# Kernel optimization log

Measured on AMD Instinct MI355X. Metric: run time of the kernel, lower is better.

Reference implementation:

```python
import jax, jax.numpy as jnp
import numpy as np

N = 100000
E = 1600000
IN_CH = 128
HID = 128
HEADS = 4
C = HID // HEADS  # 32 per-head channels
NUM_CLASSES = 40
NEG_SLOPE = 0.2


def _glorot(key, shape):
    fan_in, fan_out = shape[0], shape[-1]
    lim = jnp.sqrt(6.0 / (fan_in + fan_out))
    return jax.random.uniform(key, shape, jnp.float32, -lim, lim)


def setup_inputs() -> dict:
    key = jax.random.key(0)
    ks = jax.random.split(key, 12)
    x = jax.random.normal(ks[0], (N, IN_CH), jnp.float32)
    edge_index = jax.random.randint(ks[1], (2, E), 0, N, jnp.int64)
    edge_weight = jax.random.uniform(ks[2], (E,), jnp.float32)
    return {
        'x': x,
        'edge_index': edge_index,
        'edge_weight': edge_weight,
        'W_pre': _glorot(ks[3], (IN_CH, HID)),
        'Wl': _glorot(ks[4], (HID, HEADS * C)),
        'bl': jnp.zeros((HEADS * C,), jnp.float32),
        'Wr': _glorot(ks[5], (HID, HEADS * C)),
        'br': jnp.zeros((HEADS * C,), jnp.float32),
        'We': _glorot(ks[6], (1, HEADS * C)),
        'att': _glorot(ks[7], (HEADS, C)),
        'b_gat': jnp.zeros((HEADS * C,), jnp.float32),
        'W1': _glorot(ks[8], (HID, HID)),
        'b1': jnp.zeros((HID,), jnp.float32),
        'W2': _glorot(ks[9], (HID, NUM_CLASSES)),
        'b2': jnp.zeros((NUM_CLASSES,), jnp.float32),
    }


def reference(x, edge_index, edge_weight, W_pre, Wl, bl, Wr, br, We, att, b_gat, W1, b1, W2, b2):
    # pre projection (bias=False), norm = Identity
    h0 = x @ W_pre  # [N, HID]

    # --- GATv2Conv (PyG semantics, eval mode) ---
    # add self loops; self-loop edge_attr = mean of existing edge_attr (fill_value='mean')
    loop = jnp.arange(N, dtype=edge_index.dtype)
    src = jnp.concatenate([edge_index[0], loop])  # [E+N]
    dst = jnp.concatenate([edge_index[1], loop])
    ea = jnp.concatenate([edge_weight, jnp.full((N,), jnp.mean(edge_weight), edge_weight.dtype)])  # [E+N]

    x_l = (h0 @ Wl + bl).reshape(N, HEADS, C)  # source transform
    x_r = (h0 @ Wr + br).reshape(N, HEADS, C)  # target transform
    edge_emb = (ea[:, None] * We).reshape(-1, HEADS, C)  # lin_edge (bias=False)

    xj = x_l[src]  # [Etot, H, C] gather of source features
    e = jax.nn.leaky_relu(xj + x_r[dst] + edge_emb, NEG_SLOPE)
    alpha = jnp.einsum('ehc,hc->eh', e, att)  # [Etot, H]

    # segment softmax over destination neighborhoods
    amax = jax.ops.segment_max(alpha, dst, num_segments=N)
    amax = jnp.where(jnp.isfinite(amax), amax, 0.0)
    ex = jnp.exp(alpha - amax[dst])
    denom = jax.ops.segment_sum(ex, dst, num_segments=N)
    attn = ex / (denom[dst] + 1e-16)  # [Etot, H]

    out = jax.ops.segment_sum(attn[:, :, None] * xj, dst, num_segments=N)  # [N, H, C]
    out = out.reshape(N, HEADS * C) + b_gat

    h1 = jax.nn.elu(out)
    h = h0 + h1  # residual

    logits = jax.nn.relu(h @ W1 + b1) @ W2 + b2
    return h, logits
```

## Files before the change

### kernel.cpp

```cpp
#include <hip/hip_runtime.h>

typedef __attribute__((ext_vector_type(8))) short short8;
typedef __attribute__((ext_vector_type(16))) float f32x16;

#if __has_builtin(__builtin_amdgcn_exp2f)
#define EXP2(x) __builtin_amdgcn_exp2f(x)
#else
#define EXP2(x) exp2f(x)
#endif

static __device__ __forceinline__ unsigned short f2bf(float f){
  unsigned u = __float_as_uint(f);
  unsigned r = u + 0x7fffu + ((u >> 16) & 1u);
  return (unsigned short)(r >> 16);
}
static __device__ __forceinline__ float bf2f(unsigned short h){
  return __uint_as_float(((unsigned)h) << 16);
}

__global__ void wprep(const float* __restrict__ Wpre, const float* __restrict__ W1,
                      const float* __restrict__ W2, const float* __restrict__ bl,
                      const float* __restrict__ br,
                      unsigned short* __restrict__ PhiF, unsigned short* __restrict__ PloF,
                      unsigned short* __restrict__ W1hiF, unsigned short* __restrict__ W1loF,
                      unsigned short* __restrict__ W2hiF, unsigned short* __restrict__ W2loF,
                      float* __restrict__ bcat){
  int i = blockIdx.x*256 + threadIdx.x;
  float v; unsigned short* hp; unsigned short* lp; size_t idx;
  if (i < 16384){
    int k = i >> 7, c = i & 127;
    v = Wpre[i]; hp = PhiF; lp = PloF;
    idx = ((size_t)(k>>3)*128 + c)*8 + (k&7);
  } else if (i < 32768){
    int j = i - 16384; int k = j >> 7, c = j & 127;
    v = W1[j]; hp = W1hiF; lp = W1loF;
    idx = ((size_t)(k>>3)*128 + c)*8 + (k&7);
  } else if (i < 37888){
    int j = i - 32768; int k = j / 40, c = j % 40;
    v = W2[j]; hp = W2hiF; lp = W2loF;
    idx = ((size_t)(k>>3)*40 + c)*8 + (k&7);
  } else if (i < 38144){
    int j = i - 37888;
    bcat[j] = (j < 128) ? bl[j] : br[j-128];
    return;
  } else return;
  unsigned short h = f2bf(v);
  hp[idx] = h;
  lp[idx] = f2bf(v - bf2f(h));
}

__global__ __launch_bounds__(256) void wcomb_kernel(
    const float* __restrict__ Wpre, const float* __restrict__ Wl,
    const float* __restrict__ Wr,
    unsigned short* __restrict__ ChiF, unsigned short* __restrict__ CloF){
  int tid = blockIdx.x*256 + threadIdx.x;
  int r = tid >> 8;
  int c = tid & 255;
  const float* B = (c < 128) ? (Wl + c) : (Wr + (c - 128));
  float s = 0.f;
  for (int k = 0; k < 128; ++k)
    s = fmaf(Wpre[r*128 + k], B[(size_t)k*128], s);
  unsigned short h = f2bf(s);
  size_t idx = ((size_t)(r>>3)*256 + c)*8 + (r&7);
  ChiF[idx] = h;
  CloF[idx] = f2bf(s - bf2f(h));
}

__global__ void count_mean(const int* __restrict__ ei, const float* __restrict__ ew,
                           int* __restrict__ deg, int* __restrict__ rk,
                           float* __restrict__ msum, int E){
  float s = 0.f;
  for (int e = blockIdx.x*256 + threadIdx.x; e < E; e += gridDim.x*256){
    rk[e] = atomicAdd(&deg[ei[E + e]], 1);
    s += ew[e];
  }
  for (int d = 32; d > 0; d >>= 1) s += __shfl_down(s, d, 64);
  __shared__ float ps[4];
  int lane = threadIdx.x & 63, w = threadIdx.x >> 6;
  if (lane == 0) ps[w] = s;
  __syncthreads();
  if (threadIdx.x == 0) atomicAdd(msum, (ps[0]+ps[1]+ps[2]+ps[3]) / (float)E);
}

__global__ __launch_bounds__(256) void scan1_kernel(const int* __restrict__ deg, int* __restrict__ rowptr,
                                                    int* __restrict__ bsum, int* __restrict__ dhist, int N){
  __shared__ int s[256];
  __shared__ int lhist[256];
  int i = blockIdx.x*256 + threadIdx.x;
  lhist[threadIdx.x] = 0;
  __syncthreads();
  int v = (i < N) ? deg[i] : 0;
  if (i < N) atomicAdd(&lhist[v < 255 ? v : 255], 1);
  s[threadIdx.x] = v;
  __syncthreads();
  for (int off = 1; off < 256; off <<= 1){
    int t = (threadIdx.x >= off) ? s[threadIdx.x - off] : 0;
    __syncthreads();
    s[threadIdx.x] += t;
    __syncthreads();
  }
  if (i < N) rowptr[i + 1] = s[threadIdx.x];
  if (threadIdx.x == 255) bsum[blockIdx.x] = s[255];
  int c = lhist[threadIdx.x];
  if (c > 0) atomicAdd(&dhist[threadIdx.x], c);
}

__global__ __launch_bounds__(512) void scan2_kernel(const int* __restrict__ bsum, int* __restrict__ boff, int nb,
                                                    const int* __restrict__ dhist, int* __restrict__ dhoff){
  __shared__ int s[512];
  __shared__ int s2[256];
  int v = (threadIdx.x < nb) ? bsum[threadIdx.x] : 0;
  s[threadIdx.x] = v;
  __syncthreads();
  for (int off = 1; off < 512; off <<= 1){
    int t = (threadIdx.x >= off) ? s[threadIdx.x - off] : 0;
    __syncthreads();
    s[threadIdx.x] += t;
    __syncthreads();
  }
  if (threadIdx.x < nb) boff[threadIdx.x] = s[threadIdx.x] - v;
  int v2 = 0;
  if (threadIdx.x < 256){ v2 = dhist[threadIdx.x]; s2[threadIdx.x] = v2; }
  __syncthreads();
  for (int off = 1; off < 256; off <<= 1){
    int t = 0;
    if (threadIdx.x < 256 && threadIdx.x >= off) t = s2[threadIdx.x - off];
    __syncthreads();
    if (threadIdx.x < 256) s2[threadIdx.x] += t;
    __syncthreads();
  }
  if (threadIdx.x < 256) dhoff[threadIdx.x] = s2[threadIdx.x] - v2;
}

__global__ __launch_bounds__(256) void scan3_kernel(int* __restrict__ rowptr, const int* __restrict__ boff,
                                                    const int* __restrict__ deg, int* __restrict__ dhoff,
                                                    int* __restrict__ perm, int N){
  __shared__ int lcnt[256];
  __shared__ int lbase[256];
  int i = blockIdx.x*256 + threadIdx.x;
  lcnt[threadIdx.x] = 0;
  __syncthreads();
  if (i == 0) rowptr[0] = 0;
  int d = 0, lr = 0;
  if (i < N){
    rowptr[i + 1] += boff[i >> 8];
    d = deg[i]; d = d < 255 ? d : 255;
    lr = atomicAdd(&lcnt[d], 1);
  }
  __syncthreads();
  int c = lcnt[threadIdx.x];
  if (c > 0) lbase[threadIdx.x] = atomicAdd(&dhoff[threadIdx.x], c);
  __syncthreads();
  if (i < N) perm[lbase[d] + lr] = i;
}

__global__ void fill_kernel(const int* __restrict__ ei, const float* __restrict__ ew,
                            const int* __restrict__ rowptr, const int* __restrict__ rk,
                            int2* __restrict__ erec, int E){
  int e = blockIdx.x*256 + threadIdx.x;
  if (e >= E) return;
  int dst = ei[E + e];
  erec[rowptr[dst] + rk[e]] = make_int2(ei[e], __float_as_int(ew[e]));
}

template<int NT>
static __device__ __forceinline__ void stageA(short* alds, const float* __restrict__ A,
                                              int row0, int N, int t){
  for (int g = t; g < 1024; g += NT){
    int r = g >> 4, k8 = g & 15;
    int grow = row0 + r;
    float4 p0, p1;
    if (grow < N){
      const float* ap = A + (size_t)grow*128 + k8*8;
      p0 = *(const float4*)ap;
      p1 = *(const float4*)(ap + 4);
    } else {
      p0 = make_float4(0.f,0.f,0.f,0.f); p1 = p0;
    }
    float vv[8] = {p0.x,p0.y,p0.z,p0.w,p1.x,p1.y,p1.z,p1.w};
    short8 hv, lv;
    #pragma unroll
    for (int j = 0; j < 8; ++j){
      unsigned short h = f2bf(vv[j]);
      hv[j] = (short)h;
      lv[j] = (short)f2bf(vv[j] - bf2f(h));
    }
    int slot = k8 ^ (r & 15);
    *(short8*)&alds[r*128 + slot*8] = hv;
    *(short8*)&alds[8192 + r*128 + slot*8] = lv;
  }
}

#define MFMA_KLOOP(ACC0, ACC1) \
  _Pragma("unroll") \
  for (int ks = 0; ks < 8; ++ks){ \
    int k8 = ks*2 + kg; \
    const short* a0 = &alds[r0*128 + (k8 ^ sx)*8]; \
    const short* a1 = &alds[(r0+32)*128 + (k8 ^ sx)*8]; \
    short8 a0h = *(const short8*)a0; \
    short8 a0l = *(const short8*)(a0 + 8192); \
    short8 a1h = *(const short8*)a1; \
    short8 a1l = *(const short8*)(a1 + 8192); \
    ACC0 = __builtin_amdgcn_mfma_f32_32x32x16_bf16(a0h, bh[ks],  ACC0, 0,0,0); \
    ACC1 = __builtin_amdgcn_mfma_f32_32x32x16_bf16(a1h, bh[ks],  ACC1, 0,0,0); \
    ACC0 = __builtin_amdgcn_mfma_f32_32x32x16_bf16(a0l, bh[ks],  ACC0, 0,0,0); \
    ACC1 = __builtin_amdgcn_mfma_f32_32x32x16_bf16(a1l, bh[ks],  ACC1, 0,0,0); \
    ACC0 = __builtin_amdgcn_mfma_f32_32x32x16_bf16(a0h, bl8[ks], ACC0, 0,0,0); \
    ACC1 = __builtin_amdgcn_mfma_f32_32x32x16_bf16(a1h, bl8[ks], ACC1, 0,0,0); \
  }

__global__ __launch_bounds__(768) void pre_kernel(
    const float* __restrict__ A,
    const unsigned short* __restrict__ PhiF, const unsigned short* __restrict__ PloF,
    const unsigned short* __restrict__ ChiF, const unsigned short* __restrict__ CloF,
    const float* __restrict__ bcat,
    float* __restrict__ hout, unsigned short* __restrict__ xlr, int N, int ntiles)
{
  __shared__ short sh[2][16384];
  const int t = threadIdx.x;
  const int lane = t & 63, w = t >> 6;
  const int cl = lane & 31, kg = lane >> 5;
  const int sx = cl & 15;
  const int S = w * 32;
  const bool isP = S < 128;
  const int col = isP ? (S + cl) : (S - 128 + cl);
  const int NC  = isP ? 128 : 256;
  const unsigned short* Bhi = isP ? PhiF : ChiF;
  const unsigned short* Blo = isP ? PloF : CloF;
  const float bv = isP ? 0.f : bcat[col];

  short8 bh[8], bl8[8];
  #pragma unroll
  for (int ks = 0; ks < 8; ++ks){
    size_t off = ((size_t)(ks*2 + kg)*NC + col)*8;
    bh[ks]  = *(const short8*)(Bhi + off);
    bl8[ks] = *(const short8*)(Blo + off);
  }

  const int r_0 = t >> 4,         k8_0 = t & 15;
  const int g1  = t + 768;
  const int r_1 = g1 >> 4,        k8_1 = g1 & 15;
  const bool has1 = g1 < 1024;
  float4 pa0, pa1, pb0, pb1;

  auto LOAD = [&](int tl){
    int row0 = tl*64;
    int gr = row0 + r_0;
    if (gr < N){ const float* ap = A + (size_t)gr*128 + k8_0*8; pa0 = *(const float4*)ap; pa1 = *(const float4*)(ap+4); }
    else { pa0 = make_float4(0.f,0.f,0.f,0.f); pa1 = pa0; }
    if (has1){
      int gr1 = row0 + r_1;
      if (gr1 < N){ const float* ap = A + (size_t)gr1*128 + k8_1*8; pb0 = *(const float4*)ap; pb1 = *(const float4*)(ap+4); }
      else { pb0 = make_float4(0.f,0.f,0.f,0.f); pb1 = pb0; }
    }
  };
  auto STORE = [&](short* buf){
    {
      float vv[8] = {pa0.x,pa0.y,pa0.z,pa0.w,pa1.x,pa1.y,pa1.z,pa1.w};
      short8 hv, lv;
      #pragma unroll
      for (int j = 0; j < 8; ++j){
        unsigned short h = f2bf(vv[j]);
        hv[j] = (short)h;
        lv[j] = (short)f2bf(vv[j] - bf2f(h));
      }
      int slot = k8_0 ^ (r_0 & 15);
      *(short8*)&buf[r_0*128 + slot*8] = hv;
      *(short8*)&buf[8192 + r_0*128 + slot*8] = lv;
    }
    if (has1){
      float vv[8] = {pb0.x,pb0.y,pb0.z,pb0.w,pb1.x,pb1.y,pb1.z,pb1.w};
      short8 hv, lv;
      #pragma unroll
      for (int j = 0; j < 8; ++j){
        unsigned short h = f2bf(vv[j]);
        hv[j] = (short)h;
        lv[j] = (short)f2bf(vv[j] - bf2f(h));
      }
      int slot = k8_1 ^ (r_1 & 15);
      *(short8*)&buf[r_1*128 + slot*8] = hv;
      *(short8*)&buf[8192 + r_1*128 + slot*8] = lv;
    }
  };
  auto COMPUTE = [&](int tl, const short* alds){
    f32x16 acc0, acc1;
    #pragma unroll
    for (int i = 0; i < 16; ++i){ acc0[i] = 0.f; acc1[i] = 0.f; }
    const int r0 = cl;
    MFMA_KLOOP(acc0, acc1)
    int row0 = tl*64;
    if (isP){
      #pragma unroll
      for (int rt2 = 0; rt2 < 2; ++rt2){
        const f32x16& ac = rt2 ? acc1 : acc0;
        #pragma unroll
        for (int reg = 0; reg < 16; ++reg){
          int row = rt2*32 + (reg & 3) + 8*(reg >> 2) + 4*kg;
          int grow = row0 + row;
          if (grow < N) hout[(size_t)grow*128 + col] = ac[reg];
        }
      }
    } else {
      #pragma unroll
      for (int rt2 = 0; rt2 < 2; ++rt2){
        const f32x16& ac = rt2 ? acc1 : acc0;
        #pragma unroll
        for (int reg = 0; reg < 16; ++reg){
          int row = rt2*32 + (reg & 3) + 8*(reg >> 2) + 4*kg;
          int grow = row0 + row;
          if (grow < N) xlr[(size_t)grow*256 + col] = f2bf(ac[reg] + bv);
        }
      }
    }
  };

  int tile = blockIdx.x;
  if (tile >= ntiles) return;
  LOAD(tile);
  STORE(sh[0]);
  __syncthreads();
  int cur = 0;
  while (true){
    int next = tile + gridDim.x;
    bool more = next < ntiles;
    if (more) LOAD(next);
    COMPUTE(tile, sh[cur]);
    if (!more) break;
    STORE(sh[cur^1]);
    __syncthreads();
    cur ^= 1;
    tile = next;
  }
}

__global__ __launch_bounds__(256) void mlp_kernel(
    const float* __restrict__ A,
    const unsigned short* __restrict__ B1hi, const unsigned short* __restrict__ B1lo,
    const float* __restrict__ b1,
    const unsigned short* __restrict__ B2hi, const unsigned short* __restrict__ B2lo,
    const float* __restrict__ b2,
    float* __restrict__ logits, int N)
{
  __shared__ short alds[2*64*128];
  const int t = threadIdx.x;
  const int row0 = blockIdx.x * 64;
  stageA<256>(alds, A, row0, N, t);
  __syncthreads();

  const int lane = t & 63, w = t >> 6;
  const int cl = lane & 31, kg = lane >> 5;
  const int r0 = cl;
  const int sx = r0 & 15;

  {
    const int col = w*32 + cl;
    short8 bh[8], bl8[8];
    #pragma unroll
    for (int ks = 0; ks < 8; ++ks){
      size_t off = ((size_t)(ks*2 + kg)*128 + col)*8;
      bh[ks]  = *(const short8*)(B1hi + off);
      bl8[ks] = *(const short8*)(B1lo + off);
    }
    f32x16 acc0, acc1;
    #pragma unroll
    for (int i = 0; i < 16; ++i){ acc0[i] = 0.f; acc1[i] = 0.f; }
    MFMA_KLOOP(acc0, acc1)

    float bv = b1[col];
    __syncthreads();
    #pragma unroll
    for (int rt = 0; rt < 2; ++rt){
      const f32x16& ac = rt ? acc1 : acc0;
      #pragma unroll
      for (int reg = 0; reg < 16; ++reg){
        int row = rt*32 + (reg & 3) + 8*(reg >> 2) + 4*kg;
        float v = fmaxf(ac[reg] + bv, 0.f);
        unsigned short h = f2bf(v);
        unsigned short l = f2bf(v - bf2f(h));
        int idx = row*128 + (((col >> 3) ^ (row & 15)) << 3) + (col & 7);
        alds[idx] = (short)h;
        alds[8192 + idx] = (short)l;
      }
    }
    __syncthreads();
  }

  if (w < 2){
    const int col = w*32 + cl;
    const bool cok = col < 40;
    short8 bh[8], bl8[8];
    #pragma unroll
    for (int ks = 0; ks < 8; ++ks){
      if (cok){
        size_t off = ((size_t)(ks*2 + kg)*40 + col)*8;
        bh[ks]  = *(const short8*)(B2hi + off);
        bl8[ks] = *(const short8*)(B2lo + off);
      } else {
        #pragma unroll
        for (int j = 0; j < 8; ++j){ bh[ks][j] = 0; bl8[ks][j] = 0; }
      }
    }
    f32x16 acc0, acc1;
    #pragma unroll
    for (int i = 0; i < 16; ++i){ acc0[i] = 0.f; acc1[i] = 0.f; }
    MFMA_KLOOP(acc0, acc1)

    if (cok){
      float bv = b2[col];
      #pragma unroll
      for (int rt = 0; rt < 2; ++rt){
        const f32x16& ac = rt ? acc1 : acc0;
        #pragma unroll
        for (int reg = 0; reg < 16; ++reg){
          int row = rt*32 + (reg & 3) + 8*(reg >> 2) + 4*kg;
          int grow = row0 + row;
          if (grow < N) logits[(size_t)grow*40 + col] = ac[reg] + bv;
        }
      }
    }
  }
}

__global__ __launch_bounds__(256) void gather_kernel(
    const int* __restrict__ rowptr, const int2* __restrict__ erec,
    const unsigned short* __restrict__ xlr,
    const int* __restrict__ perm,
    const float* __restrict__ We, const float* __restrict__ att,
    const float* __restrict__ msum, const float* __restrict__ bgat,
    float* __restrict__ hbuf, int N)
{
  const int wid  = threadIdx.x >> 6;
  const int lane = threadIdx.x & 63;
  const int g    = lane >> 4;
  const int l    = lane & 15;
  const int ch0  = l * 8;
  const int slot = (blockIdx.x*4 + wid)*4 + g;
  const bool nok = slot < N;
  const int n    = nok ? perm[slot] : 0;

  float xrv[8], wev[8], at6[8], at4[8];
  {
    short8 q = *(const short8*)&xlr[(size_t)n*256 + 128 + ch0];
    float4 w0 = *(const float4*)&We[ch0];
    float4 w1 = *(const float4*)&We[ch0+4];
    float4 a0 = *(const float4*)&att[ch0];
    float4 a1 = *(const float4*)&att[ch0+4];
    const float L2E = 1.4426950408889634f;
    float wv[8] = {w0.x,w0.y,w0.z,w0.w,w1.x,w1.y,w1.z,w1.w};
    float av[8] = {a0.x,a0.y,a0.z,a0.w,a1.x,a1.y,a1.z,a1.w};
    #pragma unroll
    for (int j = 0; j < 8; ++j){
      xrv[j] = bf2f((unsigned short)q[j]);
      wev[j] = wv[j];
      at6[j] = av[j]*0.6f*L2E;
      at4[j] = av[j]*0.4f*L2E;
    }
  }

  float num[8];
  #pragma unroll
  for (int j = 0; j < 8; ++j) num[j] = 0.f;
  float den = 0.f;

  const float wm = msum[0];
  int beg = 0, end = 0;
  if (nok){ beg = rowptr[n]; end = rowptr[n + 1]; }
  const int cnt = nok ? (end - beg + 1) : 0;

  int itMax = cnt;
  itMax = max(itMax, __shfl_xor(itMax, 16, 64));
  itMax = max(itMax, __shfl_xor(itMax, 32, 64));

  const int2 selfrec = make_int2(n, __float_as_int(wm));

  int pos = beg;
  int2 rec0 = (pos     < end) ? erec[pos]     : selfrec;
  int2 rec1 = (pos + 1 < end) ? erec[pos + 1] : selfrec;
  int2 rec2 = (pos + 2 < end) ? erec[pos + 2] : selfrec;
  short8 pv0 = *(const short8*)&xlr[(size_t)rec0.x*256 + ch0];
  short8 pv1 = *(const short8*)&xlr[(size_t)rec1.x*256 + ch0];
  short8 pv2 = *(const short8*)&xlr[(size_t)rec2.x*256 + ch0];

  for (int it = 0; it < itMax; it += 2){
    int2 rec3 = (pos + 3 < end) ? erec[pos + 3] : selfrec;
    int2 rec4 = (pos + 4 < end) ? erec[pos + 4] : selfrec;
    short8 pv3 = *(const short8*)&xlr[(size_t)rec3.x*256 + ch0];
    short8 pv4 = *(const short8*)&xlr[(size_t)rec4.x*256 + ch0];

    {
      const bool act = it < cnt;
      const float wj = __int_as_float(rec0.y);
      float xlv[8];
      #pragma unroll
      for (int q = 0; q < 8; ++q) xlv[q] = bf2f((unsigned short)pv0[q]);
      float p = 0.f;
      #pragma unroll
      for (int q = 0; q < 8; ++q){
        float z = fmaf(wj, wev[q], xlv[q] + xrv[q]);
        p = fmaf(at6[q], z, p);
        p = fmaf(at4[q], fabsf(z), p);
      }
      p += __shfl_xor(p, 1, 64);
      p += __shfl_xor(p, 2, 64);
      float ex = act ? EXP2(p) : 0.f;
      den += ex;
      #pragma unroll
      for (int q = 0; q < 8; ++q) num[q] = fmaf(ex, xlv[q], num[q]);
    }
    {
      const bool act = (it + 1) < cnt;
      const float wj = __int_as_float(rec1.y);
      float xlv[8];
      #pragma unroll
      for (int q = 0; q < 8; ++q) xlv[q] = bf2f((unsigned short)pv1[q]);
      float p = 0.f;
      #pragma unroll
      for (int q = 0; q < 8; ++q){
        float z = fmaf(wj, wev[q], xlv[q] + xrv[q]);
        p = fmaf(at6[q], z, p);
        p = fmaf(at4[q], fabsf(z), p);
      }
      p += __shfl_xor(p, 1, 64);
      p += __shfl_xor(p, 2, 64);
      float ex = act ? EXP2(p) : 0.f;
      den += ex;
      #pragma unroll
      for (int q = 0; q < 8; ++q) num[q] = fmaf(ex, xlv[q], num[q]);
    }

    rec0 = rec2; rec1 = rec3; rec2 = rec4;
    pv0 = pv2;  pv1 = pv3;  pv2 = pv4;
    pos += 2;
  }

  if (nok){
    float inv = 1.f / (den + 1e-16f);
    float o[8];
    #pragma unroll
    for (int j = 0; j < 8; ++j){
      float v = num[j]*inv + bgat[ch0+j];
      o[j] = v > 0.f ? v : expm1f(v);
    }
    float4 h0a = *(const float4*)&hbuf[(size_t)n*128 + ch0];
    float4 h0b = *(const float4*)&hbuf[(size_t)n*128 + ch0 + 4];
    h0a.x += o[0]; h0a.y += o[1]; h0a.z += o[2]; h0a.w += o[3];
    h0b.x += o[4]; h0b.y += o[5]; h0b.z += o[6]; h0b.w += o[7];
    *(float4*)&hbuf[(size_t)n*128 + ch0]     = h0a;
    *(float4*)&hbuf[(size_t)n*128 + ch0 + 4] = h0b;
  }
}

extern "C" void kernel_launch(void* const* d_in, const int* in_sizes, int n_in,
                              void* d_out, int out_size, void* d_ws, size_t ws_size,
                              hipStream_t stream)
{
  const float* x    = (const float*)d_in[0];
  const int*   ei   = (const int*)  d_in[1];
  const float* ew   = (const float*)d_in[2];
  const float* Wpre = (const float*)d_in[3];
  const float* Wl   = (const float*)d_in[4];
  const float* bl   = (const float*)d_in[5];
  const float* Wr   = (const float*)d_in[6];
  const float* br   = (const float*)d_in[7];
  const float* We   = (const float*)d_in[8];
  const float* att  = (const float*)d_in[9];
  const float* bgat = (const float*)d_in[10];
  const float* W1   = (const float*)d_in[11];
  const float* b1   = (const float*)d_in[12];
  const float* W2   = (const float*)d_in[13];
  const float* b2   = (const float*)d_in[14];

  const int N = in_sizes[0] / 128;
  const int E = in_sizes[2];
  const int nb = (N + 255) / 256;

  float* hout   = (float*)d_out;
  float* logits = hout + (size_t)N*128;

  unsigned short* xlr = (unsigned short*)d_ws;
  int2*  erec   = (int2*)(xlr + (size_t)N*256);
  int*   rk     = (int*)(erec + E);
  int*   rowptr = rk + E;
  int*   cursor = rowptr + N + 1;
  float* msum   = (float*)(cursor + N);
  int*   dhist  = (int*)(msum + 1);
  int*   bsum   = dhist + 256;
  int*   boff   = bsum + nb;
  int*   dhoff  = boff + nb;
  int*   perm   = dhoff + 256;
  float* bcat   = (float*)(perm + N);
  unsigned short* wsp = (unsigned short*)(((uintptr_t)(bcat + 256) + 15) & ~(uintptr_t)15);
  unsigned short* PhiF  = wsp;
  unsigned short* PloF  = PhiF + 16384;
  unsigned short* ChiF  = PloF + 16384;
  unsigned short* CloF  = ChiF + 32768;
  unsigned short* W1hiF = CloF + 32768;
  unsigned short* W1loF = W1hiF + 16384;
  unsigned short* W2hiF = W1loF + 16384;
  unsigned short* W2loF = W2hiF + 5120;

  hipMemsetAsync(cursor, 0, (size_t)(N + 1 + 256) * sizeof(int), stream);

  wprep<<<150, 256, 0, stream>>>(Wpre, W1, W2, bl, br,
                                 PhiF, PloF, W1hiF, W1loF, W2hiF, W2loF, bcat);
  wcomb_kernel<<<128, 256, 0, stream>>>(Wpre, Wl, Wr, ChiF, CloF);
  count_mean<<<1024, 256, 0, stream>>>(ei, ew, cursor, rk, msum, E);
  scan1_kernel<<<nb, 256, 0, stream>>>(cursor, rowptr, bsum, dhist, N);
  scan2_kernel<<<1, 512, 0, stream>>>(bsum, boff, nb, dhist, dhoff);
  scan3_kernel<<<nb, 256, 0, stream>>>(rowptr, boff, cursor, dhoff, perm, N);
  fill_kernel<<<(E + 255)/256, 256, 0, stream>>>(ei, ew, rowptr, rk, erec, E);

  const int ntiles = (N + 63) / 64;
  pre_kernel<<<512, 768, 0, stream>>>(x, PhiF, PloF, ChiF, CloF, bcat, hout, xlr, N, ntiles);

  gather_kernel<<<(N + 15)/16, 256, 0, stream>>>(rowptr, erec, xlr, perm, We, att, msum, bgat, hout, N);

  mlp_kernel<<<(N + 63)/64, 256, 0, stream>>>(hout, W1hiF, W1loF, b1, W2hiF, W2loF, b2, logits, N);
}
```

Baseline: 299.3 us.

## Merge weight prep kernels, persist MLP kernel, reverse gather node order

Merges the wprep and wcomb weight-preparation kernels into one launch, which saves one kernel launch. Turns the MLP kernel into a persistent grid of 512 blocks that loops over tiles, so the W1/W2 fragments are loaded into registers once per block instead of once per tile. The gather kernel now reads the degree-sorted permutation in reverse order, which changes which nodes are scheduled first and so may improve load balance. The persistent MLP adds register pressure, because both B1 and B2 fragments stay live, and it adds an extra barrier per tile.

```diff
diff --git a/kernel.cpp b/kernel.cpp
--- a/kernel.cpp
+++ b/kernel.cpp
@@ -18,52 +18,52 @@
   return __uint_as_float(((unsigned)h) << 16);
 }
 
-__global__ void wprep(const float* __restrict__ Wpre, const float* __restrict__ W1,
-                      const float* __restrict__ W2, const float* __restrict__ bl,
-                      const float* __restrict__ br,
-                      unsigned short* __restrict__ PhiF, unsigned short* __restrict__ PloF,
-                      unsigned short* __restrict__ W1hiF, unsigned short* __restrict__ W1loF,
-                      unsigned short* __restrict__ W2hiF, unsigned short* __restrict__ W2loF,
-                      float* __restrict__ bcat){
-  int i = blockIdx.x*256 + threadIdx.x;
-  float v; unsigned short* hp; unsigned short* lp; size_t idx;
-  if (i < 16384){
-    int k = i >> 7, c = i & 127;
-    v = Wpre[i]; hp = PhiF; lp = PloF;
-    idx = ((size_t)(k>>3)*128 + c)*8 + (k&7);
-  } else if (i < 32768){
-    int j = i - 16384; int k = j >> 7, c = j & 127;
-    v = W1[j]; hp = W1hiF; lp = W1loF;
-    idx = ((size_t)(k>>3)*128 + c)*8 + (k&7);
-  } else if (i < 37888){
-    int j = i - 32768; int k = j / 40, c = j % 40;
-    v = W2[j]; hp = W2hiF; lp = W2loF;
-    idx = ((size_t)(k>>3)*40 + c)*8 + (k&7);
-  } else if (i < 38144){
-    int j = i - 37888;
-    bcat[j] = (j < 128) ? bl[j] : br[j-128];
-    return;
-  } else return;
-  unsigned short h = f2bf(v);
-  hp[idx] = h;
-  lp[idx] = f2bf(v - bf2f(h));
-}
-
-__global__ __launch_bounds__(256) void wcomb_kernel(
+__global__ __launch_bounds__(256) void wprep(
     const float* __restrict__ Wpre, const float* __restrict__ Wl,
-    const float* __restrict__ Wr,
-    unsigned short* __restrict__ ChiF, unsigned short* __restrict__ CloF){
-  int tid = blockIdx.x*256 + threadIdx.x;
-  int r = tid >> 8;
-  int c = tid & 255;
-  const float* B = (c < 128) ? (Wl + c) : (Wr + (c - 128));
-  float s = 0.f;
-  for (int k = 0; k < 128; ++k)
-    s = fmaf(Wpre[r*128 + k], B[(size_t)k*128], s);
-  unsigned short h = f2bf(s);
-  size_t idx = ((size_t)(r>>3)*256 + c)*8 + (r&7);
-  ChiF[idx] = h;
-  CloF[idx] = f2bf(s - bf2f(h));
+    const float* __restrict__ Wr, const float* __restrict__ W1,
+    const float* __restrict__ W2, const float* __restrict__ bl,
+    const float* __restrict__ br,
+    unsigned short* __restrict__ PhiF, unsigned short* __restrict__ PloF,
+    unsigned short* __restrict__ ChiF, unsigned short* __restrict__ CloF,
+    unsigned short* __restrict__ W1hiF, unsigned short* __restrict__ W1loF,
+    unsigned short* __restrict__ W2hiF, unsigned short* __restrict__ W2loF,
+    float* __restrict__ bcat){
+  if (blockIdx.x < 150){
+    int i = blockIdx.x*256 + threadIdx.x;
+    float v; unsigned short* hp; unsigned short* lp; size_t idx;
+    if (i < 16384){
+      int k = i >> 7, c = i & 127;
+      v = Wpre[i]; hp = PhiF; lp = PloF;
+      idx = ((size_t)(k>>3)*128 + c)*8 + (k&7);
+    } else if (i < 32768){
+      int j = i - 16384; int k = j >> 7, c = j & 127;
+      v = W1[j]; hp = W1hiF; lp = W1loF;
+      idx = ((size_t)(k>>3)*128 + c)*8 + (k&7);
+    } else if (i < 37888){
+      int j = i - 32768; int k = j / 40, c = j % 40;
+      v = W2[j]; hp = W2hiF; lp = W2loF;
+      idx = ((size_t)(k>>3)*40 + c)*8 + (k&7);
+    } else if (i < 38144){
+      int j = i - 37888;
+      bcat[j] = (j < 128) ? bl[j] : br[j-128];
+      return;
+    } else return;
+    unsigned short h = f2bf(v);
+    hp[idx] = h;
+    lp[idx] = f2bf(v - bf2f(h));
+  } else {
+    int tid = (blockIdx.x - 150)*256 + threadIdx.x;
+    int r = tid >> 8;
+    int c = tid & 255;
+    const float* B = (c < 128) ? (Wl + c) : (Wr + (c - 128));
+    float s = 0.f;
+    for (int k = 0; k < 128; ++k)
+      s = fmaf(Wpre[r*128 + k], B[(size_t)k*128], s);
+    unsigned short h = f2bf(s);
+    size_t idx = ((size_t)(r>>3)*256 + c)*8 + (r&7);
+    ChiF[idx] = h;
+    CloF[idx] = f2bf(s - bf2f(h));
+  }
 }
 
 __global__ void count_mean(const int* __restrict__ ei, const float* __restrict__ ew,
@@ -191,7 +191,7 @@
   }
 }
 
-#define MFMA_KLOOP(ACC0, ACC1) \
+#define MFMA_KLOOP(ACC0, ACC1, BH, BL) \
   _Pragma("unroll") \
   for (int ks = 0; ks < 8; ++ks){ \
     int k8 = ks*2 + kg; \
@@ -201,12 +201,12 @@
     short8 a0l = *(const short8*)(a0 + 8192); \
     short8 a1h = *(const short8*)a1; \
     short8 a1l = *(const short8*)(a1 + 8192); \
-    ACC0 = __builtin_amdgcn_mfma_f32_32x32x16_bf16(a0h, bh[ks],  ACC0, 0,0,0); \
-    ACC1 = __builtin_amdgcn_mfma_f32_32x32x16_bf16(a1h, bh[ks],  ACC1, 0,0,0); \
-    ACC0 = __builtin_amdgcn_mfma_f32_32x32x16_bf16(a0l, bh[ks],  ACC0, 0,0,0); \
-    ACC1 = __builtin_amdgcn_mfma_f32_32x32x16_bf16(a1l, bh[ks],  ACC1, 0,0,0); \
-    ACC0 = __builtin_amdgcn_mfma_f32_32x32x16_bf16(a0h, bl8[ks], ACC0, 0,0,0); \
-    ACC1 = __builtin_amdgcn_mfma_f32_32x32x16_bf16(a1h, bl8[ks], ACC1, 0,0,0); \
+    ACC0 = __builtin_amdgcn_mfma_f32_32x32x16_bf16(a0h, BH[ks], ACC0, 0,0,0); \
+    ACC1 = __builtin_amdgcn_mfma_f32_32x32x16_bf16(a1h, BH[ks], ACC1, 0,0,0); \
+    ACC0 = __builtin_amdgcn_mfma_f32_32x32x16_bf16(a0l, BH[ks], ACC0, 0,0,0); \
+    ACC1 = __builtin_amdgcn_mfma_f32_32x32x16_bf16(a1l, BH[ks], ACC1, 0,0,0); \
+    ACC0 = __builtin_amdgcn_mfma_f32_32x32x16_bf16(a0h, BL[ks], ACC0, 0,0,0); \
+    ACC1 = __builtin_amdgcn_mfma_f32_32x32x16_bf16(a1h, BL[ks], ACC1, 0,0,0); \
   }
 
 __global__ __launch_bounds__(768) void pre_kernel(
@@ -237,9 +237,9 @@
     bl8[ks] = *(const short8*)(Blo + off);
   }
 
-  const int r_0 = t >> 4,         k8_0 = t & 15;
+  const int r_0 = t >> 4,  k8_0 = t & 15;
   const int g1  = t + 768;
-  const int r_1 = g1 >> 4,        k8_1 = g1 & 15;
+  const int r_1 = g1 >> 4, k8_1 = g1 & 15;
   const bool has1 = g1 < 1024;
   float4 pa0, pa1, pb0, pb1;
 
@@ -287,7 +287,7 @@
     #pragma unroll
     for (int i = 0; i < 16; ++i){ acc0[i] = 0.f; acc1[i] = 0.f; }
     const int r0 = cl;
-    MFMA_KLOOP(acc0, acc1)
+    MFMA_KLOOP(acc0, acc1, bh, bl8)
     int row0 = tl*64;
     if (isP){
       #pragma unroll
@@ -339,82 +339,85 @@
     const float* __restrict__ b1,
     const unsigned short* __restrict__ B2hi, const unsigned short* __restrict__ B2lo,
     const float* __restrict__ b2,
-    float* __restrict__ logits, int N)
+    float* __restrict__ logits, int N, int ntiles)
 {
   __shared__ short alds[2*64*128];
   const int t = threadIdx.x;
-  const int row0 = blockIdx.x * 64;
-  stageA<256>(alds, A, row0, N, t);
-  __syncthreads();
-
   const int lane = t & 63, w = t >> 6;
   const int cl = lane & 31, kg = lane >> 5;
-  const int r0 = cl;
-  const int sx = r0 & 15;
-
-  {
-    const int col = w*32 + cl;
-    short8 bh[8], bl8[8];
-    #pragma unroll
-    for (int ks = 0; ks < 8; ++ks){
-      size_t off = ((size_t)(ks*2 + kg)*128 + col)*8;
-      bh[ks]  = *(const short8*)(B1hi + off);
-      bl8[ks] = *(const short8*)(B1lo + off);
-    }
-    f32x16 acc0, acc1;
-    #pragma unroll
-    for (int i = 0; i < 16; ++i){ acc0[i] = 0.f; acc1[i] = 0.f; }
-    MFMA_KLOOP(acc0, acc1)
-
-    float bv = b1[col];
-    __syncthreads();
-    #pragma unroll
-    for (int rt = 0; rt < 2; ++rt){
-      const f32x16& ac = rt ? acc1 : acc0;
-      #pragma unroll
-      for (int reg = 0; reg < 16; ++reg){
-        int row = rt*32 + (reg & 3) + 8*(reg >> 2) + 4*kg;
-        float v = fmaxf(ac[reg] + bv, 0.f);
-        unsigned short h = f2bf(v);
-        unsigned short l = f2bf(v - bf2f(h));
-        int idx = row*128 + (((col >> 3) ^ (row & 15)) << 3) + (col & 7);
-        alds[idx] = (short)h;
-        alds[8192 + idx] = (short)l;
-      }
-    }
-    __syncthreads();
-  }
-
-  if (w < 2){
-    const int col = w*32 + cl;
-    const bool cok = col < 40;
-    short8 bh[8], bl8[8];
-    #pragma unroll
-    for (int ks = 0; ks < 8; ++ks){
-      if (cok){
-        size_t off = ((size_t)(ks*2 + kg)*40 + col)*8;
-        bh[ks]  = *(const short8*)(B2hi + off);
-        bl8[ks] = *(const short8*)(B2lo + off);
-      } else {
-        #pragma unroll
-        for (int j = 0; j < 8; ++j){ bh[ks][j] = 0; bl8[ks][j] = 0; }
-      }
-    }
-    f32x16 acc0, acc1;
-    #pragma unroll
-    for (int i = 0; i < 16; ++i){ acc0[i] = 0.f; acc1[i] = 0.f; }
-    MFMA_KLOOP(acc0, acc1)
-
+  const int sx = cl & 15;
+  const int col = w*32 + cl;
+
+  short8 b1h[8], b1l[8];
+  #pragma unroll
+  for (int ks = 0; ks < 8; ++ks){
+    size_t off = ((size_t)(ks*2 + kg)*128 + col)*8;
+    b1h[ks] = *(const short8*)(B1hi + off);
+    b1l[ks] = *(const short8*)(B1lo + off);
+  }
+  const float bv1 = b1[col];
+
+  const bool cok = (w < 2) && (col < 40);
+  short8 b2h[8], b2l[8];
+  #pragma unroll
+  for (int ks = 0; ks < 8; ++ks){
     if (cok){
-      float bv = b2[col];
+      size_t off = ((size_t)(ks*2 + kg)*40 + col)*8;
+      b2h[ks] = *(const short8*)(B2hi + off);
+      b2l[ks] = *(const short8*)(B2lo + off);
+    } else {
+      #pragma unroll
+      for (int j = 0; j < 8; ++j){ b2h[ks][j] = 0; b2l[ks][j] = 0; }
+    }
+  }
+  const float bv2 = cok ? b2[col] : 0.f;
+
+  for (int tile = blockIdx.x; tile < ntiles; tile += gridDim.x){
+    __syncthreads();
+    stageA<256>(alds, A, tile*64, N, t);
+    __syncthreads();
+
+    {
+      f32x16 acc0, acc1;
+      #pragma unroll
+      for (int i = 0; i < 16; ++i){ acc0[i] = 0.f; acc1[i] = 0.f; }
+      const int r0 = cl;
+      MFMA_KLOOP(acc0, acc1, b1h, b1l)
+      __syncthreads();
       #pragma unroll
       for (int rt = 0; rt < 2; ++rt){
         const f32x16& ac = rt ? acc1 : acc0;
         #pragma unroll
         for (int reg = 0; reg < 16; ++reg){
           int row = rt*32 + (reg & 3) + 8*(reg >> 2) + 4*kg;
-          int grow = row0 + row;
-          if (grow < N) logits[(size_t)grow*40 + col] = ac[reg] + bv;
+          float v = fmaxf(ac[reg] + bv1, 0.f);
+          unsigned short h = f2bf(v);
+          unsigned short l = f2bf(v - bf2f(h));
+          int idx = row*128 + (((col >> 3) ^ (row & 15)) << 3) + (col & 7);
+          alds[idx] = (short)h;
+          alds[8192 + idx] = (short)l;
+        }
+      }
+      __syncthreads();
+    }
+
+    if (w < 2){
+      f32x16 acc0, acc1;
+      #pragma unroll
+      for (int i = 0; i < 16; ++i){ acc0[i] = 0.f; acc1[i] = 0.f; }
+      const int r0 = cl;
+      MFMA_KLOOP(acc0, acc1, b2h, b2l)
+      if (cok){
+        int row0 = tile*64;
+        #pragma unroll
+        for (int rt = 0; rt < 2; ++rt){
+          const f32x16& ac = rt ? acc1 : acc0;
+          #pragma unroll
+          for (int reg = 0; reg < 16; ++reg){
+            int row = rt*32 + (reg & 3) + 8*(reg >> 2) + 4*kg;
+            int grow = row0 + row;
+            if (grow < N) logits[(size_t)grow*40 + col] = ac[reg] + bv2;
+          }
         }
       }
     }
@@ -436,7 +439,7 @@
   const int ch0  = l * 8;
   const int slot = (blockIdx.x*4 + wid)*4 + g;
   const bool nok = slot < N;
-  const int n    = nok ? perm[slot] : 0;
+  const int n    = nok ? perm[N-1-slot] : 0;
 
   float xrv[8], wev[8], at6[8], at4[8];
   {
@@ -601,9 +604,8 @@
 
   hipMemsetAsync(cursor, 0, (size_t)(N + 1 + 256) * sizeof(int), stream);
 
-  wprep<<<150, 256, 0, stream>>>(Wpre, W1, W2, bl, br,
-                                 PhiF, PloF, W1hiF, W1loF, W2hiF, W2loF, bcat);
-  wcomb_kernel<<<128, 256, 0, stream>>>(Wpre, Wl, Wr, ChiF, CloF);
+  wprep<<<278, 256, 0, stream>>>(Wpre, Wl, Wr, W1, W2, bl, br,
+                                 PhiF, PloF, ChiF, CloF, W1hiF, W1loF, W2hiF, W2loF, bcat);
   count_mean<<<1024, 256, 0, stream>>>(ei, ew, cursor, rk, msum, E);
   scan1_kernel<<<nb, 256, 0, stream>>>(cursor, rowptr, bsum, dhist, N);
   scan2_kernel<<<1, 512, 0, stream>>>(bsum, boff, nb, dhist, dhoff);
@@ -615,5 +617,5 @@
 
   gather_kernel<<<(N + 15)/16, 256, 0, stream>>>(rowptr, erec, xlr, perm, We, att, msum, bgat, hout, N);
 
-  mlp_kernel<<<(N + 63)/64, 256, 0, stream>>>(hout, W1hiF, W1loF, b1, W2hiF, W2loF, b2, logits, N);
-}
+  mlp_kernel<<<512, 256, 0, stream>>>(hout, W1hiF, W1loF, b1, W2hiF, W2loF, b2, logits, N, ntiles);
+}
```

Measured after the change: 294.7 us. No clear change (-1.5%).
